# Kernel optimization log

Hardware: AMD Instinct MI355X
Metric: run time of the kernel (lower is better)

Reference implementation:

```python
import jax, jax.numpy as jnp
import numpy as np

N = 100000   # nodes in batched graph
E = 1600000  # edges
B = 2048     # number of user/item pairs (target links)
IN = 4       # one-hot node label dim
H = 32       # latent dim per layer
R = 5        # num relations (rating levels)
NB = 2       # num bases
L = 4        # num conv layers


def setup_inputs() -> dict:
    key = jax.random.key(0)
    ks = jax.random.split(key, 16)
    s = 0.1
    # node labels: first B nodes are users (class 0), next B items (class 1), rest hop labels {2,3}
    cls = jax.random.randint(ks[0], (N,), 2, IN)
    cls = cls.at[:B].set(0).at[B:2 * B].set(1)
    x = jax.nn.one_hot(cls, IN, dtype=jnp.float32)
    src = jax.random.randint(ks[1], (E,), 0, N)
    dst = jax.random.randint(ks[2], (E,), 0, N)
    etype = jax.random.randint(ks[3], (E,), 0, R)
    V0 = jax.random.normal(ks[4], (NB, IN, H), jnp.float32) * s
    comp0 = jax.random.normal(ks[5], (R, NB), jnp.float32) * s
    loop0 = jax.random.normal(ks[6], (IN, H), jnp.float32) * s
    bias0 = jnp.zeros((H,), jnp.float32)
    Vs = jax.random.normal(ks[7], (L - 1, NB, H, H), jnp.float32) * s
    comps = jax.random.normal(ks[8], (L - 1, R, NB), jnp.float32) * s
    loops = jax.random.normal(ks[9], (L - 1, H, H), jnp.float32) * s
    biases = jnp.zeros((L - 1, H), jnp.float32)
    w1 = jax.random.normal(ks[10], (128, 2 * L * H), jnp.float32) * 0.05
    b1 = jnp.zeros((128,), jnp.float32)
    w2 = jax.random.normal(ks[11], (1, 128), jnp.float32) * 0.05
    b2 = jnp.zeros((1,), jnp.float32)
    return {"x": x, "src": src, "dst": dst, "etype": etype,
            "V0": V0, "comp0": comp0, "loop0": loop0, "bias0": bias0,
            "Vs": Vs, "comps": comps, "loops": loops, "biases": biases,
            "w1": w1, "b1": b1, "w2": w2, "b2": b2}


def _rgcn(h, src, dst, etype, V, comp, loopW, bias):
    # basis-decomposed RelGraphConv: W_r = sum_b comp[r,b] * V[b]
    # precompute per-basis transforms at nodes, then combine per edge by relation coeff
    xb = jnp.einsum('ni,bio->nbo', h, V)            # [N, NB, out]
    m = jnp.einsum('eb,ebo->eo', comp[etype], xb[src])  # [E, out]
    agg = jax.ops.segment_sum(m, dst, num_segments=h.shape[0])  # sum aggregation
    return agg + h @ loopW + bias                   # self-loop + bias


def reference(x, src, dst, etype, V0, comp0, loop0, bias0, Vs, comps, loops, biases, w1, b1, w2, b2):
    states = []
    h = jnp.tanh(_rgcn(x, src, dst, etype, V0, comp0, loop0, bias0))
    states.append(h)
    for i in range(L - 1):
        h = jnp.tanh(_rgcn(h, src, dst, etype, Vs[i], comps[i], loops[i], biases[i]))
        states.append(h)
    cs = jnp.concatenate(states, axis=1)            # [N, L*H]
    # users are nodes [0,B), items are nodes [B,2B) by construction (x[:,0]==1 / x[:,1]==1)
    feat = jnp.concatenate([cs[:B], cs[B:2 * B]], axis=1)  # [B, 2*L*H]
    hid = jax.nn.relu(feat @ w1.T + b1)             # dropout inactive (eval)
    out = (hid @ w2.T + b2)[:, 0] * 1               # multiply_by = 1
    return out
```

## Files before the change

kernel.cpp:

```cpp
#include <hip/hip_runtime.h>
#include <hip/hip_fp16.h>

constexpr int N_  = 100000;
constexpr int E_  = 1600000;
constexpr int B_  = 2048;
constexpr int NT_ = 2 * B_;

constexpr int NPB_SHIFT = 9;
constexpr int NPB = 1 << NPB_SHIFT;
constexpr int KB_ = (N_ + NPB - 1) / NPB;
constexpr int CAP_ = 9216;
constexpr int PCHUNK = 8192;
constexpr int NPBLK = (E_ + PCHUNK - 1) / PCHUNK;

__global__ __launch_bounds__(256) void init_kernel(
    const float* __restrict__ x, const float* __restrict__ w1,
    unsigned char* __restrict__ cls, int* __restrict__ flag,
    int* __restrict__ cnt, int* __restrict__ bcur, float* __restrict__ w1t)
{
    const int b = blockIdx.x, t = threadIdx.x;
    if (b < 391) {
        const int n = b * 256 + t;
        if (n < N_) {
            const float4 v = *(const float4*)(x + n * 4);
            cls[n] = v.y > 0.5f ? 1 : (v.z > 0.5f ? 2 : (v.w > 0.5f ? 3 : 0));
            flag[n] = 0;
        }
        if (b == 0 && t == 0) *cnt = 0;
    } else if (b < 519) {
        const int idx = (b - 391) * 256 + t;
        const int j = idx >> 8, k = idx & 255;
        w1t[k * 128 + j] = w1[idx];
    } else {
        if (t < KB_) bcur[t] = 0;
    }
}

__global__ __launch_bounds__(256) void partition_kernel(
    const int* __restrict__ src, const int* __restrict__ dst,
    const int* __restrict__ etype, int* __restrict__ bcur, int* __restrict__ ebuf)
{
    __shared__ int hist[KB_];
    __shared__ int gbase[KB_];
    __shared__ int lcur[KB_];
    const int t = threadIdx.x;
    for (int i = t; i < KB_; i += 256) { hist[i] = 0; lcur[i] = 0; }
    __syncthreads();
    const int e0 = blockIdx.x * PCHUNK;
    const int e1 = min(e0 + PCHUNK, E_);
    for (int i = e0 + t; i < e1; i += 256) atomicAdd(&hist[dst[i] >> NPB_SHIFT], 1);
    __syncthreads();
    for (int i = t; i < KB_; i += 256) if (hist[i]) gbase[i] = atomicAdd(&bcur[i], hist[i]);
    __syncthreads();
    for (int i = e0 + t; i < e1; i += 256) {
        const int d = dst[i];
        const int b = d >> NPB_SHIFT;
        const int lp = atomicAdd(&lcur[b], 1);
        ebuf[(size_t)b * CAP_ + gbase[b] + lp] = src[i] | (etype[i] << 17) | ((d & (NPB - 1)) << 20);
    }
}

__global__ __launch_bounds__(512) void bfinish_kernel(
    const int* __restrict__ bcur, const int* __restrict__ ebuf,
    const unsigned char* __restrict__ cls,
    const float* __restrict__ comp0, const float* __restrict__ V0,
    const float* __restrict__ loop0, const float* __restrict__ bias0,
    int* __restrict__ rowptr, int* __restrict__ pack,
    float* __restrict__ cs, __half* __restrict__ hout,
    int* __restrict__ flag, int* __restrict__ cnt_g, int* __restrict__ nlist)
{
    const int b = blockIdx.x, t = threadIdx.x;
    if (b >= KB_) {
        const int tb = b - KB_;
        const int s0 = tb * CAP_;
        const int s1 = s0 + bcur[tb];
        const int nbase = tb << NPB_SHIFT;
        for (int nn = nbase + t; nn < nbase + NPB; nn += 512)
            nlist[atomicAdd(cnt_g, 1)] = nn;
        for (int i = s0 + t; i < s1; i += 512) {
            const int s = ebuf[i] & 0x1FFFF;
            if (s >= NT_ && atomicExch(&flag[s], 1) == 0)
                nlist[atomicAdd(cnt_g, 1)] = s;
        }
        return;
    }
    __shared__ int cnt[NPB];
    __shared__ int sh[NPB];
    __shared__ unsigned int hist[NPB * 20];
    __shared__ float sLoop[128], sV0[256], sBias[32], sCmp[10];
    cnt[t] = 0;
    for (int i = t; i < NPB * 20; i += 512) hist[i] = 0u;
    if (t < 128) sLoop[t] = loop0[t];
    if (t < 256) sV0[t]   = V0[t];
    if (t < 32)  sBias[t] = bias0[t];
    if (t < 10)  sCmp[t]  = comp0[t];
    if (t < 256) sh[t] = (t < KB_) ? bcur[t] : 0;
    __syncthreads();
#pragma unroll
    for (int off = 1; off < 256; off <<= 1) {
        int u = 0;
        if (t < 256 && t >= off) u = sh[t - off];
        __syncthreads();
        if (t < 256) sh[t] += u;
        __syncthreads();
    }
    const int myCnt = bcur[b];
    const int db = sh[b] - myCnt;
    const int s0 = b * CAP_;
    const int s1 = s0 + myCnt;
    __syncthreads();
    for (int i = s0 + t; i < s1; i += 512) {
        const int p = ebuf[i];
        const int dloc = p >> 20;
        const int et = (p >> 17) & 7;
        const int c = cls[p & 0x1FFFF];
        atomicAdd(&cnt[dloc], 1);
        atomicAdd(&hist[dloc * 20 + et * 4 + c], 1u);
    }
    __syncthreads();
    const int v = cnt[t];
    sh[t] = v; __syncthreads();
#pragma unroll
    for (int off = 1; off < NPB; off <<= 1) {
        const int u = (t >= off) ? sh[t - off] : 0;
        __syncthreads();
        sh[t] += u;
        __syncthreads();
    }
    const int rp = db + sh[t] - v;
    const int node = (b << NPB_SHIFT) + t;
    if (node < N_) rowptr[node] = rp;
    cnt[t] = rp;
    if (b == 0 && t == 0) rowptr[N_] = E_;
    __syncthreads();
    for (int i = s0 + t; i < s1; i += 512) {
        const int p = ebuf[i];
        const int pos = atomicAdd(&cnt[p >> 20], 1);
        pack[pos] = p & 0xFFFFF;
    }
    if (node < N_) {
        float A0[4], A1[4];
#pragma unroll
        for (int j = 0; j < 4; ++j) {
            float a0 = 0.f, a1 = 0.f;
#pragma unroll
            for (int r = 0; r < 5; ++r) {
                const float c = (float)hist[t * 20 + r * 4 + j];
                a0 += c * sCmp[r * 2];
                a1 += c * sCmp[r * 2 + 1];
            }
            A0[j] = a0; A1[j] = a1;
        }
        const int myc = cls[node];
        __half hrow[32];
        const bool wcs = node < NT_;
#pragma unroll 8
        for (int d = 0; d < 32; ++d) {
            float o = sBias[d] + sLoop[myc * 32 + d];
#pragma unroll
            for (int j = 0; j < 4; ++j)
                o += A0[j] * sV0[j * 32 + d] + A1[j] * sV0[128 + j * 32 + d];
            const float r = tanhf(o);
            hrow[d] = __float2half(r);
            if (wcs) cs[node * 128 + d] = r;
        }
        uint4* dst4 = (uint4*)(hout + (size_t)node * 32);
        const uint4* src4 = (const uint4*)hrow;
        dst4[0] = src4[0]; dst4[1] = src4[1]; dst4[2] = src4[2]; dst4[3] = src4[3];
    }
}

__device__ __forceinline__ void acc_chunk(
    const uint4& v, int pq, bool ok, const __half2* __restrict__ cmp2,
    __half2* h0, __half2* h1)
{
    const int tt = (pq >> 17) & 7;
    const __half2 z = __float2half2_rn(0.f);
    const __half2 c0 = ok ? cmp2[tt * 2]     : z;
    const __half2 c1 = ok ? cmp2[tt * 2 + 1] : z;
    const __half2* hp = (const __half2*)&v;
#pragma unroll
    for (int k = 0; k < 4; ++k) {
        h0[k] = __hfma2(c0, hp[k], h0[k]);
        h1[k] = __hfma2(c1, hp[k], h1[k]);
    }
}

__device__ __forceinline__ float gather_body(
    int n, int lane, int g,
    const __half* __restrict__ hin, const int* __restrict__ rowptr,
    const int* __restrict__ pack, const __half2* __restrict__ cmp2,
    const float* __restrict__ V, const float* __restrict__ loopW,
    const float* __restrict__ bias, float (*hs)[96])
{
    hs[g][lane] = __half2float(hin[n * 32 + lane]);
    const int beg = rowptr[n], end = rowptr[n + 1];
    const int sg = lane >> 2;
    const int c  = lane & 3;
    const int i0 = beg + sg, i1 = i0 + 8, i2 = i0 + 16, i3 = i0 + 24;
    const int p0 = pack[i0 < end ? i0 : beg];
    const int p1 = pack[i1 < end ? i1 : beg];
    const int p2 = pack[i2 < end ? i2 : beg];
    const int p3 = pack[i3 < end ? i3 : beg];
    const uint4 v0 = *(const uint4*)(hin + (size_t)(p0 & 0x1FFFF) * 32 + c * 8);
    const uint4 v1 = *(const uint4*)(hin + (size_t)(p1 & 0x1FFFF) * 32 + c * 8);
    const uint4 v2 = *(const uint4*)(hin + (size_t)(p2 & 0x1FFFF) * 32 + c * 8);
    const uint4 v3 = *(const uint4*)(hin + (size_t)(p3 & 0x1FFFF) * 32 + c * 8);
    __half2 h0[4], h1[4];
    const __half2 z = __float2half2_rn(0.f);
#pragma unroll
    for (int k = 0; k < 4; ++k) { h0[k] = z; h1[k] = z; }
    acc_chunk(v0, p0, i0 < end, cmp2, h0, h1);
    acc_chunk(v1, p1, i1 < end, cmp2, h0, h1);
    acc_chunk(v2, p2, i2 < end, cmp2, h0, h1);
    acc_chunk(v3, p3, i3 < end, cmp2, h0, h1);
    for (int e0 = beg + 32; e0 < end; e0 += 8) {
        const int e = e0 + sg;
        const bool ok = e < end;
        const int p = pack[ok ? e : beg];
        const uint4 u = *(const uint4*)(hin + (size_t)(p & 0x1FFFF) * 32 + c * 8);
        acc_chunk(u, p, ok, cmp2, h0, h1);
    }
    float a0[8], a1[8];
#pragma unroll
    for (int k = 0; k < 4; ++k) {
        const float2 f0 = __half22float2(h0[k]);
        const float2 f1 = __half22float2(h1[k]);
        a0[2 * k] = f0.x; a0[2 * k + 1] = f0.y;
        a1[2 * k] = f1.x; a1[2 * k + 1] = f1.y;
    }
#pragma unroll
    for (int k = 0; k < 8; ++k) {
        a0[k] += __shfl_xor(a0[k], 4);
        a0[k] += __shfl_xor(a0[k], 8);
        a0[k] += __shfl_xor(a0[k], 16);
        a1[k] += __shfl_xor(a1[k], 4);
        a1[k] += __shfl_xor(a1[k], 8);
        a1[k] += __shfl_xor(a1[k], 16);
    }
    if (lane < 4) {
#pragma unroll
        for (int k = 0; k < 8; ++k) {
            hs[g][32 + c * 8 + k] = a0[k];
            hs[g][64 + c * 8 + k] = a1[k];
        }
    }
    __builtin_amdgcn_wave_barrier();
    float o = bias[lane];
#pragma unroll 8
    for (int k = 0; k < 32; ++k) {
        o += hs[g][k] * loopW[k * 32 + lane]
           + hs[g][32 + k] * V[k * 32 + lane]
           + hs[g][64 + k] * V[1024 + k * 32 + lane];
    }
    return tanhf(o);
}

__global__ __launch_bounds__(256) void gather_kernel(
    const __half* __restrict__ hin, const int* __restrict__ rowptr,
    const int* __restrict__ pack, const float* __restrict__ comp,
    const float* __restrict__ V, const float* __restrict__ loopW,
    const float* __restrict__ bias,
    float* __restrict__ cs, __half* __restrict__ hout, int out_off)
{
    __shared__ float hs[8][96];
    __shared__ __half2 cmp2[10];
    const int t = threadIdx.x, lane = t & 31, g = t >> 5;
    if (lane < 10) cmp2[lane] = __float2half2_rn(comp[lane]);
    __builtin_amdgcn_wave_barrier();
    const int n = blockIdx.x * 8 + g;
    const float r = gather_body(n, lane, g, hin, rowptr, pack, cmp2, V, loopW, bias, hs);
    if (n < NT_) cs[n * 128 + out_off + lane] = r;
    hout[n * 32 + lane] = __float2half(r);
}

__global__ __launch_bounds__(256) void gatherL_kernel(
    const __half* __restrict__ hin, const int* __restrict__ rowptr,
    const int* __restrict__ pack, const float* __restrict__ comp,
    const float* __restrict__ V, const float* __restrict__ loopW,
    const float* __restrict__ bias,
    const int* __restrict__ nlist, const int* __restrict__ cnt,
    float* __restrict__ cs, __half* __restrict__ hout, int out_off)
{
    __shared__ float hs[8][96];
    __shared__ __half2 cmp2[10];
    const int t = threadIdx.x, lane = t & 31, g = t >> 5;
    if (lane < 10) cmp2[lane] = __float2half2_rn(comp[lane]);
    __builtin_amdgcn_wave_barrier();
    const int idx = blockIdx.x * 8 + g;
    if (idx >= *cnt) return;
    const int n = nlist[idx];
    const float r = gather_body(n, lane, g, hin, rowptr, pack, cmp2, V, loopW, bias, hs);
    if (n < NT_) cs[n * 128 + out_off + lane] = r;
    hout[n * 32 + lane] = __float2half(r);
}

__global__ __launch_bounds__(128) void mlp_kernel(
    const __half* __restrict__ hin, const int* __restrict__ rowptr,
    const int* __restrict__ pack, const float* __restrict__ comp,
    const float* __restrict__ V, const float* __restrict__ loopW,
    const float* __restrict__ bias,
    const float* __restrict__ cs, const float* __restrict__ w1t,
    const float* __restrict__ b1, const float* __restrict__ w2,
    const float* __restrict__ b2, float* __restrict__ out)
{
    __shared__ float feat[256];
    __shared__ float hs[2][96];
    __shared__ __half2 cmp2[10];
    __shared__ float part[2];
    const int p = blockIdx.x, t = threadIdx.x;
    if (t < 10) cmp2[t] = __float2half2_rn(comp[t]);
    if (t < 64) {
        const int g = t >> 5, lane = t & 31;
        const int n = g ? (B_ + p) : p;
        const float r = gather_body(n, lane, g, hin, rowptr, pack, cmp2, V, loopW, bias, hs);
        feat[g * 128 + 96 + lane] = r;
    } else {
        const int i = t - 64;
        for (int j = i; j < 96; j += 64) {
            feat[j]       = cs[p * 128 + j];
            feat[128 + j] = cs[(B_ + p) * 128 + j];
        }
    }
    __syncthreads();
    float acc = b1[t];
#pragma unroll 8
    for (int k = 0; k < 256; ++k) acc += feat[k] * w1t[k * 128 + t];
    const float hid = acc > 0.f ? acc : 0.f;
    float v = w2[t] * hid;
#pragma unroll
    for (int off = 32; off > 0; off >>= 1) v += __shfl_down(v, off, 64);
    if ((t & 63) == 0) part[t >> 6] = v;
    __syncthreads();
    if (t == 0) out[p] = part[0] + part[1] + b2[0];
}

extern "C" void kernel_launch(void* const* d_in, const int* in_sizes, int n_in,
                              void* d_out, int out_size, void* d_ws, size_t ws_size,
                              hipStream_t stream) {
    const float* x      = (const float*)d_in[0];
    const int*   src    = (const int*)d_in[1];
    const int*   dst    = (const int*)d_in[2];
    const int*   etype  = (const int*)d_in[3];
    const float* V0     = (const float*)d_in[4];
    const float* comp0  = (const float*)d_in[5];
    const float* loop0  = (const float*)d_in[6];
    const float* bias0  = (const float*)d_in[7];
    const float* Vs     = (const float*)d_in[8];
    const float* comps  = (const float*)d_in[9];
    const float* loops  = (const float*)d_in[10];
    const float* biases = (const float*)d_in[11];
    const float* w1     = (const float*)d_in[12];
    const float* b1     = (const float*)d_in[13];
    const float* w2     = (const float*)d_in[14];
    const float* b2     = (const float*)d_in[15];
    float* out = (float*)d_out;

    float* ws   = (float*)d_ws;
    float* cs   = ws;
    float* w1t  = cs + (size_t)NT_ * 128;
    __half* hA  = (__half*)(w1t + 256 * 128);
    __half* hB  = hA + (size_t)N_ * 32;
    int* ebuf   = (int*)(hB + (size_t)N_ * 32);
    int* pack   = ebuf + (size_t)KB_ * CAP_;
    int* rowptr = pack + E_;
    int* flag   = rowptr + N_ + 1;
    int* cnt    = flag + N_;
    int* nlist  = cnt + 1;
    int* bcur   = nlist + N_;
    unsigned char* cls = (unsigned char*)(bcur + KB_);

    const int gathBlocks = N_ / 8;

    init_kernel<<<520, 256, 0, stream>>>(x, w1, cls, flag, cnt, bcur, w1t);
    partition_kernel<<<NPBLK, 256, 0, stream>>>(src, dst, etype, bcur, ebuf);
    bfinish_kernel<<<KB_ + 8, 512, 0, stream>>>(bcur, ebuf, cls, comp0, V0, loop0, bias0,
                                                rowptr, pack, cs, hA, flag, cnt, nlist);
    gather_kernel<<<gathBlocks, 256, 0, stream>>>(
        hA, rowptr, pack, comps + 0, Vs + 0, loops + 0, biases + 0, cs, hB, 32);
    gatherL_kernel<<<gathBlocks, 256, 0, stream>>>(
        hB, rowptr, pack, comps + 10, Vs + 2048, loops + 1024, biases + 32,
        nlist, cnt, cs, hA, 64);
    mlp_kernel<<<B_, 128, 0, stream>>>(
        hA, rowptr, pack, comps + 20, Vs + 4096, loops + 2048, biases + 64,
        cs, w1t, b1, w2, b2, out);
}
```

Baseline: 172.0 us.

## Transpose layer weights, aggregate in half precision, batch node-list appends

```diff
diff --git a/kernel.cpp b/kernel.cpp
--- a/kernel.cpp
+++ b/kernel.cpp
@@ -12,11 +12,14 @@
 constexpr int CAP_ = 9216;
 constexpr int PCHUNK = 8192;
 constexpr int NPBLK = (E_ + PCHUNK - 1) / PCHUNK;
+constexpr int HSTR = 21;
 
 __global__ __launch_bounds__(256) void init_kernel(
     const float* __restrict__ x, const float* __restrict__ w1,
+    const float* __restrict__ loops, const float* __restrict__ Vs,
     unsigned char* __restrict__ cls, int* __restrict__ flag,
-    int* __restrict__ cnt, int* __restrict__ bcur, float* __restrict__ w1t)
+    int* __restrict__ cnt, int* __restrict__ bcur, float* __restrict__ w1t,
+    float* __restrict__ wT)
 {
     const int b = blockIdx.x, t = threadIdx.x;
     if (b < 391) {
@@ -31,8 +34,16 @@
         const int idx = (b - 391) * 256 + t;
         const int j = idx >> 8, k = idx & 255;
         w1t[k * 128 + j] = w1[idx];
+    } else if (b == 519) {
+        if (t < KB_) bcur[t] = 0;
     } else {
-        if (t < KB_) bcur[t] = 0;
+        const int idx = (b - 520) * 256 + t;
+        const int l = idx / 3072, rem = idx % 3072;
+        const int m = rem >> 10, q = rem & 1023;
+        const int d = q >> 5, k = q & 31;
+        const float v = (m == 0) ? loops[l * 1024 + k * 32 + d]
+                                 : Vs[l * 2048 + (m - 1) * 1024 + k * 32 + d];
+        wT[idx] = v;
     }
 }
 
@@ -69,27 +80,33 @@
     float* __restrict__ cs, __half* __restrict__ hout,
     int* __restrict__ flag, int* __restrict__ cnt_g, int* __restrict__ nlist)
 {
+    __shared__ int cnt[NPB];
+    __shared__ int sh[NPB];
+    __shared__ unsigned int hist[NPB * HSTR];
+    __shared__ float sLoop[128], sV0[256], sBias[32], sCmp[10];
+    __shared__ int lcnt, gbase_s;
     const int b = blockIdx.x, t = threadIdx.x;
     if (b >= KB_) {
         const int tb = b - KB_;
         const int s0 = tb * CAP_;
         const int s1 = s0 + bcur[tb];
         const int nbase = tb << NPB_SHIFT;
-        for (int nn = nbase + t; nn < nbase + NPB; nn += 512)
-            nlist[atomicAdd(cnt_g, 1)] = nn;
+        int* lbuf = (int*)hist;
+        if (t == 0) lcnt = NPB;
+        lbuf[t] = nbase + t;
+        __syncthreads();
         for (int i = s0 + t; i < s1; i += 512) {
             const int s = ebuf[i] & 0x1FFFF;
             if (s >= NT_ && atomicExch(&flag[s], 1) == 0)
-                nlist[atomicAdd(cnt_g, 1)] = s;
-        }
+                lbuf[atomicAdd(&lcnt, 1)] = s;
+        }
+        __syncthreads();
+        if (t == 0) gbase_s = atomicAdd(cnt_g, lcnt);
+        __syncthreads();
+        for (int j = t; j < lcnt; j += 512) nlist[gbase_s + j] = lbuf[j];
         return;
     }
-    __shared__ int cnt[NPB];
-    __shared__ int sh[NPB];
-    __shared__ unsigned int hist[NPB * 20];
-    __shared__ float sLoop[128], sV0[256], sBias[32], sCmp[10];
-    cnt[t] = 0;
-    for (int i = t; i < NPB * 20; i += 512) hist[i] = 0u;
+    for (int i = t; i < NPB * HSTR; i += 512) hist[i] = 0u;
     if (t < 128) sLoop[t] = loop0[t];
     if (t < 256) sV0[t]   = V0[t];
     if (t < 32)  sBias[t] = bias0[t];
@@ -111,14 +128,13 @@
     __syncthreads();
     for (int i = s0 + t; i < s1; i += 512) {
         const int p = ebuf[i];
-        const int dloc = p >> 20;
-        const int et = (p >> 17) & 7;
-        const int c = cls[p & 0x1FFFF];
-        atomicAdd(&cnt[dloc], 1);
-        atomicAdd(&hist[dloc * 20 + et * 4 + c], 1u);
-    }
-    __syncthreads();
-    const int v = cnt[t];
+        const int et_c = ((p >> 17) & 7) * 4 + cls[p & 0x1FFFF];
+        atomicAdd(&hist[(p >> 20) * HSTR + et_c], 1u);
+    }
+    __syncthreads();
+    int v = 0;
+#pragma unroll
+    for (int j = 0; j < 20; ++j) v += (int)hist[t * HSTR + j];
     sh[t] = v; __syncthreads();
 #pragma unroll
     for (int off = 1; off < NPB; off <<= 1) {
@@ -145,7 +161,7 @@
             float a0 = 0.f, a1 = 0.f;
 #pragma unroll
             for (int r = 0; r < 5; ++r) {
-                const float c = (float)hist[t * 20 + r * 4 + j];
+                const float c = (float)hist[t * HSTR + r * 4 + j];
                 a0 += c * sCmp[r * 2];
                 a1 += c * sCmp[r * 2 + 1];
             }
@@ -190,7 +206,7 @@
     int n, int lane, int g,
     const __half* __restrict__ hin, const int* __restrict__ rowptr,
     const int* __restrict__ pack, const __half2* __restrict__ cmp2,
-    const float* __restrict__ V, const float* __restrict__ loopW,
+    const float* __restrict__ wT,
     const float* __restrict__ bias, float (*hs)[96])
 {
     hs[g][lane] = __half2float(hin[n * 32 + lane]);
@@ -221,37 +237,43 @@
         const uint4 u = *(const uint4*)(hin + (size_t)(p & 0x1FFFF) * 32 + c * 8);
         acc_chunk(u, p, ok, cmp2, h0, h1);
     }
-    float a0[8], a1[8];
-#pragma unroll
-    for (int k = 0; k < 4; ++k) {
-        const float2 f0 = __half22float2(h0[k]);
-        const float2 f1 = __half22float2(h1[k]);
-        a0[2 * k] = f0.x; a0[2 * k + 1] = f0.y;
-        a1[2 * k] = f1.x; a1[2 * k + 1] = f1.y;
-    }
-#pragma unroll
-    for (int k = 0; k < 8; ++k) {
-        a0[k] += __shfl_xor(a0[k], 4);
-        a0[k] += __shfl_xor(a0[k], 8);
-        a0[k] += __shfl_xor(a0[k], 16);
-        a1[k] += __shfl_xor(a1[k], 4);
-        a1[k] += __shfl_xor(a1[k], 8);
-        a1[k] += __shfl_xor(a1[k], 16);
+#pragma unroll
+    for (int m = 4; m <= 16; m <<= 1) {
+#pragma unroll
+        for (int k = 0; k < 4; ++k) {
+            const int r0 = __shfl_xor(__builtin_bit_cast(int, h0[k]), m, 32);
+            const int r1 = __shfl_xor(__builtin_bit_cast(int, h1[k]), m, 32);
+            h0[k] = __hadd2(h0[k], __builtin_bit_cast(__half2, r0));
+            h1[k] = __hadd2(h1[k], __builtin_bit_cast(__half2, r1));
+        }
     }
     if (lane < 4) {
 #pragma unroll
-        for (int k = 0; k < 8; ++k) {
-            hs[g][32 + c * 8 + k] = a0[k];
-            hs[g][64 + c * 8 + k] = a1[k];
+        for (int k = 0; k < 4; ++k) {
+            const float2 f0 = __half22float2(h0[k]);
+            const float2 f1 = __half22float2(h1[k]);
+            hs[g][32 + c * 8 + 2 * k]     = f0.x;
+            hs[g][32 + c * 8 + 2 * k + 1] = f0.y;
+            hs[g][64 + c * 8 + 2 * k]     = f1.x;
+            hs[g][64 + c * 8 + 2 * k + 1] = f1.y;
         }
     }
     __builtin_amdgcn_wave_barrier();
+    const float* wLoop = wT + lane * 32;
+    const float* wV0   = wT + 1024 + lane * 32;
+    const float* wV1   = wT + 2048 + lane * 32;
     float o = bias[lane];
-#pragma unroll 8
-    for (int k = 0; k < 32; ++k) {
-        o += hs[g][k] * loopW[k * 32 + lane]
-           + hs[g][32 + k] * V[k * 32 + lane]
-           + hs[g][64 + k] * V[1024 + k * 32 + lane];
+#pragma unroll
+    for (int k0 = 0; k0 < 32; k0 += 4) {
+        const float4 s  = *(const float4*)&hs[g][k0];
+        const float4 sa = *(const float4*)&hs[g][32 + k0];
+        const float4 sb = *(const float4*)&hs[g][64 + k0];
+        const float4 wl = *(const float4*)&wLoop[k0];
+        const float4 w0 = *(const float4*)&wV0[k0];
+        const float4 w1 = *(const float4*)&wV1[k0];
+        o += s.x*wl.x + s.y*wl.y + s.z*wl.z + s.w*wl.w
+           + sa.x*w0.x + sa.y*w0.y + sa.z*w0.z + sa.w*w0.w
+           + sb.x*w1.x + sb.y*w1.y + sb.z*w1.z + sb.w*w1.w;
     }
     return tanhf(o);
 }
@@ -259,8 +281,7 @@
 __global__ __launch_bounds__(256) void gather_kernel(
     const __half* __restrict__ hin, const int* __restrict__ rowptr,
     const int* __restrict__ pack, const float* __restrict__ comp,
-    const float* __restrict__ V, const float* __restrict__ loopW,
-    const float* __restrict__ bias,
+    const float* __restrict__ wT, const float* __restrict__ bias,
     float* __restrict__ cs, __half* __restrict__ hout, int out_off)
 {
     __shared__ float hs[8][96];
@@ -269,7 +290,7 @@
     if (lane < 10) cmp2[lane] = __float2half2_rn(comp[lane]);
     __builtin_amdgcn_wave_barrier();
     const int n = blockIdx.x * 8 + g;
-    const float r = gather_body(n, lane, g, hin, rowptr, pack, cmp2, V, loopW, bias, hs);
+    const float r = gather_body(n, lane, g, hin, rowptr, pack, cmp2, wT, bias, hs);
     if (n < NT_) cs[n * 128 + out_off + lane] = r;
     hout[n * 32 + lane] = __float2half(r);
 }
@@ -277,8 +298,7 @@
 __global__ __launch_bounds__(256) void gatherL_kernel(
     const __half* __restrict__ hin, const int* __restrict__ rowptr,
     const int* __restrict__ pack, const float* __restrict__ comp,
-    const float* __restrict__ V, const float* __restrict__ loopW,
-    const float* __restrict__ bias,
+    const float* __restrict__ wT, const float* __restrict__ bias,
     const int* __restrict__ nlist, const int* __restrict__ cnt,
     float* __restrict__ cs, __half* __restrict__ hout, int out_off)
 {
@@ -290,7 +310,7 @@
     const int idx = blockIdx.x * 8 + g;
     if (idx >= *cnt) return;
     const int n = nlist[idx];
-    const float r = gather_body(n, lane, g, hin, rowptr, pack, cmp2, V, loopW, bias, hs);
+    const float r = gather_body(n, lane, g, hin, rowptr, pack, cmp2, wT, bias, hs);
     if (n < NT_) cs[n * 128 + out_off + lane] = r;
     hout[n * 32 + lane] = __float2half(r);
 }
@@ -298,8 +318,7 @@
 __global__ __launch_bounds__(128) void mlp_kernel(
     const __half* __restrict__ hin, const int* __restrict__ rowptr,
     const int* __restrict__ pack, const float* __restrict__ comp,
-    const float* __restrict__ V, const float* __restrict__ loopW,
-    const float* __restrict__ bias,
+    const float* __restrict__ wT, const float* __restrict__ bias,
     const float* __restrict__ cs, const float* __restrict__ w1t,
     const float* __restrict__ b1, const float* __restrict__ w2,
     const float* __restrict__ b2, float* __restrict__ out)
@@ -313,7 +332,7 @@
     if (t < 64) {
         const int g = t >> 5, lane = t & 31;
         const int n = g ? (B_ + p) : p;
-        const float r = gather_body(n, lane, g, hin, rowptr, pack, cmp2, V, loopW, bias, hs);
+        const float r = gather_body(n, lane, g, hin, rowptr, pack, cmp2, wT, bias, hs);
         feat[g * 128 + 96 + lane] = r;
     } else {
         const int i = t - 64;
@@ -359,7 +378,8 @@
     float* ws   = (float*)d_ws;
     float* cs   = ws;
     float* w1t  = cs + (size_t)NT_ * 128;
-    __half* hA  = (__half*)(w1t + 256 * 128);
+    float* wT   = w1t + 256 * 128;
+    __half* hA  = (__half*)(wT + 3 * 3072);
     __half* hB  = hA + (size_t)N_ * 32;
     int* ebuf   = (int*)(hB + (size_t)N_ * 32);
     int* pack   = ebuf + (size_t)KB_ * CAP_;
@@ -372,16 +392,16 @@
 
     const int gathBlocks = N_ / 8;
 
-    init_kernel<<<520, 256, 0, stream>>>(x, w1, cls, flag, cnt, bcur, w1t);
+    init_kernel<<<556, 256, 0, stream>>>(x, w1, loops, Vs, cls, flag, cnt, bcur, w1t, wT);
     partition_kernel<<<NPBLK, 256, 0, stream>>>(src, dst, etype, bcur, ebuf);
     bfinish_kernel<<<KB_ + 8, 512, 0, stream>>>(bcur, ebuf, cls, comp0, V0, loop0, bias0,
                                                 rowptr, pack, cs, hA, flag, cnt, nlist);
     gather_kernel<<<gathBlocks, 256, 0, stream>>>(
-        hA, rowptr, pack, comps + 0, Vs + 0, loops + 0, biases + 0, cs, hB, 32);
+        hA, rowptr, pack, comps + 0, wT + 0, biases + 0, cs, hB, 32);
     gatherL_kernel<<<gathBlocks, 256, 0, stream>>>(
-        hB, rowptr, pack, comps + 10, Vs + 2048, loops + 1024, biases + 32,
+        hB, rowptr, pack, comps + 10, wT + 3072, biases + 32,
         nlist, cnt, cs, hA, 64);
     mlp_kernel<<<B_, 128, 0, stream>>>(
-        hA, rowptr, pack, comps + 20, Vs + 4096, loops + 2048, biases + 64,
+        hA, rowptr, pack, comps + 20, wT + 6144, biases + 64,
         cs, w1t, b1, w2, b2, out);
 }
```

New measurement: 314.7 us. 1.83x slower.
